# Kernel optimization log

Hardware: AMD Instinct MI355X
Metric: run time of the kernel (lower is better)

Reference implementation:

```python
import jax, jax.numpy as jnp
import numpy as np

D = 1024      # input_dim
H = 16        # head_num
HD = 64       # head_dim
HID = 4096    # mlp hidden
CUR = 512     # cur_seq
PREV = 512    # prev_seq (memory)
FULL = CUR + PREV
BS = 16
SCALE = 1.0 / (HD ** 0.5)


def setup_inputs() -> dict:
    key = jax.random.key(0)
    ks = jax.random.split(key, 20)
    def nrm(k, shape, s=0.02):
        return (jax.random.normal(k, shape) * s).astype(jnp.float32)
    inp = {
        "inputs": nrm(ks[0], (CUR, BS, D), 1.0),
        "pos_embedding": nrm(ks[1], (FULL, 1, D), 1.0),
        "u": nrm(ks[2], (H, HD)),
        "v": nrm(ks[3], (H, HD)),
        "memory": nrm(ks[4], (PREV, BS, D), 1.0),
        # causal mask: position i (query) may attend to j <= i + PREV; True = masked
        "mask": jnp.triu(jnp.ones((CUR, FULL), dtype=bool), k=PREV + 1)[:, :, None],
        # attention params (stored as (in, out); torch Linear applies x @ W.T + b)
        "Wkv": nrm(ks[5], (D, 2 * H * HD)), "bkv": jnp.zeros((2 * H * HD,), jnp.float32),
        "Wq": nrm(ks[6], (D, H * HD)), "bq": jnp.zeros((H * HD,), jnp.float32),
        "Wo": nrm(ks[7], (H * HD, D)), "bo": jnp.zeros((D,), jnp.float32),
        "Wp": nrm(ks[8], (D, H * HD)), "bp": jnp.zeros((H * HD,), jnp.float32),
        # layernorms
        "ln1_g": jnp.ones((D,), jnp.float32), "ln1_b": jnp.zeros((D,), jnp.float32),
        "ln2_g": jnp.ones((D,), jnp.float32), "ln2_b": jnp.zeros((D,), jnp.float32),
        # mlp (mlp_num=2): Linear(D,HID)+relu, Linear(HID,D)+relu
        "W1": nrm(ks[9], (D, HID)), "b1": jnp.zeros((HID,), jnp.float32),
        "W2": nrm(ks[10], (HID, D)), "b2": jnp.zeros((D,), jnp.float32),
        # GRU gates: stacked [Wr,Wz,Wg] and [Ur,Uz,Ug], no bias; bg init 2.0
        "g1_W": nrm(ks[11], (3, D, D)), "g1_U": nrm(ks[12], (3, D, D)),
        "g1_bg": jnp.full((D,), 2.0, jnp.float32),
        "g2_W": nrm(ks[13], (3, D, D)), "g2_U": nrm(ks[14], (3, D, D)),
        "g2_bg": jnp.full((D,), 2.0, jnp.float32),
    }
    return inp


def _layernorm(x, g, b, eps=1e-5):
    mu = jnp.mean(x, axis=-1, keepdims=True)
    var = jnp.mean(jnp.square(x - mu), axis=-1, keepdims=True)
    return (x - mu) * jax.lax.rsqrt(var + eps) * g + b


def _rel_shift(x):
    # x: (bs, head, cur, full) -> pad/reshape/slice trick of Transformer-XL
    b, h, c, f = x.shape
    xp = jnp.pad(x, ((0, 0), (0, 0), (0, 0), (1, 0)))      # (b,h,c,f+1)
    xp = xp.reshape(b, h, f + 1, c)
    return xp[:, :, 1:, :].reshape(b, h, c, f)


def _gru_gate(x, y, W, U, bg):
    # W, U: (3, D, D) for [r, z, g] gates; torch Linear => y @ W[i].T
    r = jax.nn.sigmoid(y @ W[0].T + x @ U[0].T)
    z = jax.nn.sigmoid(y @ W[1].T + x @ U[1].T - bg)
    h = jnp.tanh(y @ W[2].T + (r * x) @ U[2].T)
    return (1.0 - z) * x + z * h


def _attention_xl(x_cur, pos_emb, x_full, u, v, mask,
                  Wkv, bkv, Wq, bq, Wo, bo, Wp, bp):
    cur, bs, _ = x_cur.shape
    full = x_full.shape[0]
    kv = x_full @ Wkv + bkv                                  # (full, bs, 2*H*HD)
    key, value = jnp.split(kv, 2, axis=-1)
    query = x_cur @ Wq + bq                                  # (cur, bs, H*HD)
    r = (pos_emb @ Wp + bp).reshape(full, H, HD)             # (full, H, HD)

    key = key.reshape(full, bs, H, HD)
    value = value.reshape(full, bs, H, HD)
    query = query.reshape(cur, bs, H, HD)

    content = jnp.einsum('ibhd,jbhd->bhij', query + u, key)  # (bs,H,cur,full)
    position = jnp.einsum('ibhd,jhd->bhij', query + v, r)    # (bs,H,cur,full)
    position = _rel_shift(position)

    attn = (content + position) * SCALE
    # mask: (cur, full, 1) bool, True = masked
    m = mask[:, :, 0][None, None]                            # (1,1,cur,full)
    attn = jnp.where(m, -jnp.inf, attn)
    p = jax.nn.softmax(attn, axis=-1)

    out = jnp.einsum('bhij,jbhd->ibhd', p, value).reshape(cur, bs, H * HD)
    return out @ Wo + bo                                     # (cur, bs, D)


def reference(inputs, pos_embedding, u, v, memory, mask,
              Wkv, bkv, Wq, bq, Wo, bo, Wp, bp,
              ln1_g, ln1_b, ln2_g, ln2_b,
              W1, b1, W2, b2,
              g1_W, g1_U, g1_bg, g2_W, g2_U, g2_bg):
    prev = memory.shape[0]
    full_input = jnp.concatenate([memory, inputs], axis=0)   # (full, bs, D)
    x1 = _layernorm(full_input, ln1_g, ln1_b)
    a1 = _attention_xl(x1[prev:], pos_embedding, x1, u, v, mask,
                       Wkv, bkv, Wq, bq, Wo, bo, Wp, bp)
    a1 = jax.nn.relu(a1)                                     # dropout = identity (eval)
    o1 = _gru_gate(inputs, a1, g1_W, g1_U, g1_bg)
    x2 = _layernorm(o1, ln2_g, ln2_b)
    m2 = jax.nn.relu(jax.nn.relu(x2 @ W1 + b1) @ W2 + b2)    # mlp: act after every linear
    o2 = _gru_gate(o1, m2, g2_W, g2_U, g2_bg)
    return o2
```

## Files before the change

kernel.cpp:

```cpp
#include <hip/hip_runtime.h>
#include <stdint.h>

typedef _Float16 h16;
typedef __attribute__((ext_vector_type(8))) _Float16 f16x8;
typedef __attribute__((ext_vector_type(4))) _Float16 f16x4;
typedef __attribute__((ext_vector_type(4))) float f32x4;

enum { F_OBF = 1, F_BIAS = 2, F_RELU = 4, F_ACC = 8, F_DUAL = 16 };

#define BARRIER_MEM                                  \
  do {                                               \
    asm volatile("" ::: "memory");                   \
    __builtin_amdgcn_s_barrier();                    \
    asm volatile("" ::: "memory");                   \
  } while (0)

static __device__ __forceinline__ void gload16(const void* g, void* l) {
  __builtin_amdgcn_global_load_lds((__attribute__((address_space(1))) void*)g,
                                   (__attribute__((address_space(3))) void*)l,
                                   16, 0, 0);
}

template <int FLAGS>
__global__ __launch_bounds__(512) void gemm2_k(
    const h16* __restrict__ A, const h16* __restrict__ B,
    void* __restrict__ Cv, const float* __restrict__ bias,
    int K, int lda, int ldb, int ldc, int gm) {
  __shared__ h16 Al[2][256][64];
  __shared__ h16 Bl[2][256][64];

  const int tid = threadIdx.x, lane = tid & 63, wid = tid >> 6;
  const int wr = wid >> 2, wn = wid & 3;
  const int ar = lane & 15, q4 = lane >> 4;

  const int nwg = gridDim.x, cpx = nwg >> 3;
  const int bid = (blockIdx.x & 7) * cpx + (blockIdx.x >> 3);
  const int mx = bid % gm, ny = bid / gm;

  const h16* Ab = A + (long)mx * 256 * lda;
  const h16* Bb = B + (long)ny * 256 * ldb;

  auto stageA = [&](int buf, int half, int k0) {
#pragma unroll
    for (int l = 0; l < 2; ++l) {
      const int idx = l * 512 + tid;
      const int row = half * 128 + (idx >> 3), sl = idx & 7;
      gload16(Ab + (long)row * lda + k0 + (sl ^ (row & 7)) * 8,
              (char*)&Al[buf][0][0] + (half * 1024 + l * 512 + wid * 64) * 16);
    }
  };
  auto stageB = [&](int buf, int half, int k0) {
#pragma unroll
    for (int l = 0; l < 2; ++l) {
      const int idx = l * 512 + tid;
      const int row = half * 128 + (idx >> 3), sl = idx & 7;
      gload16(Bb + (long)row * ldb + k0 + (sl ^ (row & 7)) * 8,
              (char*)&Bl[buf][0][0] + (half * 1024 + l * 512 + wid * 64) * 16);
    }
  };

  f32x4 acc[8][4] = {};
  const int nk = K >> 6;

  stageB(0, 0, 0); stageB(0, 1, 0); stageA(0, 0, 0); stageA(0, 1, 0);
  if (nk > 1) { stageB(1, 0, 64); stageB(1, 1, 64); stageA(1, 0, 64); stageA(1, 1, 64); }
  if (nk > 1) asm volatile("s_waitcnt vmcnt(8)" ::: "memory");
  else        asm volatile("s_waitcnt vmcnt(0)" ::: "memory");
  BARRIER_MEM;

  for (int kt = 0; kt < nk; ++kt) {
    const int b = kt & 1;
    const int k2 = (kt + 2) << 6;
    const bool pf = (kt + 2) < nk;

    f16x8 a0[4][2], b0[2][2];
#pragma unroll
    for (int m = 0; m < 4; ++m) {
      const int row = wr * 128 + m * 16 + ar;
#pragma unroll
      for (int ks = 0; ks < 2; ++ks)
        a0[m][ks] = *(const f16x8*)&Al[b][row][((ks * 4 + q4) ^ (row & 7)) * 8];
    }
#pragma unroll
    for (int n = 0; n < 2; ++n) {
      const int row = wn * 64 + n * 16 + ar;
#pragma unroll
      for (int ks = 0; ks < 2; ++ks)
        b0[n][ks] = *(const f16x8*)&Bl[b][row][((ks * 4 + q4) ^ (row & 7)) * 8];
    }
    BARRIER_MEM;
    __builtin_amdgcn_s_setprio(1);
#pragma unroll
    for (int m = 0; m < 4; ++m)
#pragma unroll
      for (int n = 0; n < 2; ++n)
#pragma unroll
        for (int ks = 0; ks < 2; ++ks)
          acc[m][n] = __builtin_amdgcn_mfma_f32_16x16x32_f16(a0[m][ks], b0[n][ks], acc[m][n], 0, 0, 0);
    __builtin_amdgcn_s_setprio(0);
    BARRIER_MEM;

    f16x8 b1f[2][2];
#pragma unroll
    for (int n = 0; n < 2; ++n) {
      const int row = wn * 64 + (n + 2) * 16 + ar;
#pragma unroll
      for (int ks = 0; ks < 2; ++ks)
        b1f[n][ks] = *(const f16x8*)&Bl[b][row][((ks * 4 + q4) ^ (row & 7)) * 8];
    }
    BARRIER_MEM;
    __builtin_amdgcn_s_setprio(1);
#pragma unroll
    for (int m = 0; m < 4; ++m)
#pragma unroll
      for (int n = 0; n < 2; ++n)
#pragma unroll
        for (int ks = 0; ks < 2; ++ks)
          acc[m][n + 2] = __builtin_amdgcn_mfma_f32_16x16x32_f16(a0[m][ks], b1f[n][ks], acc[m][n + 2], 0, 0, 0);
    __builtin_amdgcn_s_setprio(0);
    BARRIER_MEM;

    f16x8 a1f[4][2];
#pragma unroll
    for (int m = 0; m < 4; ++m) {
      const int row = wr * 128 + (m + 4) * 16 + ar;
#pragma unroll
      for (int ks = 0; ks < 2; ++ks)
        a1f[m][ks] = *(const f16x8*)&Al[b][row][((ks * 4 + q4) ^ (row & 7)) * 8];
    }
    if (pf) { stageB(b, 0, k2); stageB(b, 1, k2); }
    BARRIER_MEM;
    __builtin_amdgcn_s_setprio(1);
#pragma unroll
    for (int m = 0; m < 4; ++m)
#pragma unroll
      for (int n = 0; n < 2; ++n)
#pragma unroll
        for (int ks = 0; ks < 2; ++ks)
          acc[m + 4][n] = __builtin_amdgcn_mfma_f32_16x16x32_f16(a1f[m][ks], b0[n][ks], acc[m + 4][n], 0, 0, 0);
    __builtin_amdgcn_s_setprio(0);
    BARRIER_MEM;

    if (pf) { stageA(b, 0, k2); stageA(b, 1, k2); }
    __builtin_amdgcn_s_setprio(1);
#pragma unroll
    for (int m = 0; m < 4; ++m)
#pragma unroll
      for (int n = 0; n < 2; ++n)
#pragma unroll
        for (int ks = 0; ks < 2; ++ks)
          acc[m + 4][n + 2] = __builtin_amdgcn_mfma_f32_16x16x32_f16(a1f[m][ks], b1f[n][ks], acc[m + 4][n + 2], 0, 0, 0);
    __builtin_amdgcn_s_setprio(0);
    if (pf)                 asm volatile("s_waitcnt vmcnt(8)" ::: "memory");
    else if (kt + 1 < nk)   asm volatile("s_waitcnt vmcnt(0)" ::: "memory");
    BARRIER_MEM;
  }

#pragma unroll
  for (int m = 0; m < 8; ++m) {
#pragma unroll
    for (int n = 0; n < 4; ++n) {
      const int col = ny * 256 + wn * 64 + n * 16 + ar;
      float bv1 = 0.f;
      if (FLAGS & F_BIAS) bv1 = bias[col];
#pragma unroll
      for (int r = 0; r < 4; ++r) {
        const int row = mx * 256 + wr * 128 + m * 16 + q4 * 4 + r;
        float val = acc[m][n][r] + bv1;
        if (FLAGS & F_RELU) val = fmaxf(val, 0.f);
        if constexpr ((FLAGS & F_ACC) != 0) {
          float* p = (float*)Cv + (long)row * ldc + col;
          *p = *p + val;
        } else if constexpr ((FLAGS & F_OBF) != 0) {
          ((h16*)Cv)[(long)row * ldc + col] = (h16)val;
        } else {
          ((float*)Cv)[(long)row * ldc + col] = val;
        }
      }
    }
  }
}

template <int BM, int BN, int WAVES_M, int WAVES_N, int FLAGS>
__global__ __launch_bounds__(256) void gemm_k(
    const h16* __restrict__ A, const h16* __restrict__ B,
    void* __restrict__ Cv, void* __restrict__ C2v,
    const float* __restrict__ bias, const float* __restrict__ bias2,
    int K, int lda, int ldb, int ldc,
    long sAb, long sAh, long sBb, long sBh, long sCb, long sCh) {
  constexpr int BK = 32;
  constexpr int WM = BM / WAVES_M, WN = BN / WAVES_N;
  constexpr int MF = WM / 16, NF = WN / 16;
  constexpr int LPS = BM / 64 + BN / 64;
  __shared__ h16 Al[3][BM][BK];
  __shared__ h16 Bl[3][BN][BK];

  const int tid = threadIdx.x, lane = tid & 63, wid = tid >> 6;
  const int wm = wid / WAVES_N, wn = wid % WAVES_N;
  const int z = blockIdx.z, zb = z >> 4, zh = z & 15;
  const h16* Ab = A + zb * sAb + zh * sAh + (long)blockIdx.x * BM * lda;
  const h16* Bb = B + zb * sBb + zh * sBh + (long)blockIdx.y * BN * ldb;

  const int srow = lane >> 2;
  const int skc = (((lane & 3) ^ ((lane >> 3) & 3)) * 8);

  auto stage = [&](int buf, int k0) {
#pragma unroll
    for (int t = 0; t < BM / 64; ++t) {
      const int ii = wid + t * 4;
      gload16(Ab + (long)(ii * 16 + srow) * lda + k0 + skc, &Al[buf][ii * 16][0]);
    }
#pragma unroll
    for (int t = 0; t < BN / 64; ++t) {
      const int ii = wid + t * 4;
      gload16(Bb + (long)(ii * 16 + srow) * ldb + k0 + skc, &Bl[buf][ii * 16][0]);
    }
  };

  f32x4 acc[MF][NF] = {};
  const int nk = K / BK;
  const int ar = lane & 15, ls = lane >> 4;

  stage(0, 0);
  if (nk > 1) stage(1, BK);
  for (int kt = 0; kt < nk; ++kt) {
    if (kt == nk - 1) {
      asm volatile("s_waitcnt vmcnt(0)" ::: "memory");
    } else if constexpr (LPS == 4) {
      asm volatile("s_waitcnt vmcnt(4)" ::: "memory");
    } else if constexpr (LPS == 3) {
      asm volatile("s_waitcnt vmcnt(3)" ::: "memory");
    } else {
      asm volatile("s_waitcnt vmcnt(0)" ::: "memory");
    }
    __builtin_amdgcn_s_barrier();
    asm volatile("" ::: "memory");
    if (kt + 2 < nk) stage((kt + 2) % 3, (kt + 2) * BK);
    const int cur = kt % 3;
    f16x8 af[MF], bv[NF];
#pragma unroll
    for (int m = 0; m < MF; ++m) {
      const int R = wm * WM + m * 16 + ar;
      af[m] = *(const f16x8*)&Al[cur][R][(ls ^ ((R >> 1) & 3)) * 8];
    }
#pragma unroll
    for (int n = 0; n < NF; ++n) {
      const int R = wn * WN + n * 16 + ar;
      bv[n] = *(const f16x8*)&Bl[cur][R][(ls ^ ((R >> 1) & 3)) * 8];
    }
#pragma unroll
    for (int m = 0; m < MF; ++m)
#pragma unroll
      for (int n = 0; n < NF; ++n)
        acc[m][n] = __builtin_amdgcn_mfma_f32_16x16x32_f16(af[m], bv[n], acc[m][n], 0, 0, 0);
  }

  const long coff = (long)zb * sCb + (long)zh * sCh;
#pragma unroll
  for (int m = 0; m < MF; ++m) {
#pragma unroll
    for (int n = 0; n < NF; ++n) {
      const int col = blockIdx.y * BN + wn * WN + n * 16 + ar;
      float bv1 = 0.f, bv2 = 0.f;
      if (FLAGS & F_BIAS) bv1 = bias[col];
      if (FLAGS & F_DUAL) bv2 = bias2[col];
#pragma unroll
      for (int r = 0; r < 4; ++r) {
        const int row = blockIdx.x * BM + wm * WM + m * 16 + (lane >> 4) * 4 + r;
        float val = acc[m][n][r] + bv1;
        if (FLAGS & F_RELU) val = fmaxf(val, 0.f);
        if constexpr ((FLAGS & F_ACC) != 0) {
          float* p = (float*)Cv + coff + (long)row * ldc + col;
          *p = *p + val;
        } else if constexpr ((FLAGS & F_OBF) != 0) {
          ((h16*)Cv)[coff + (long)row * ldc + col] = (h16)val;
          if constexpr ((FLAGS & F_DUAL) != 0)
            ((h16*)C2v)[coff + (long)row * ldc + col] = (h16)(acc[m][n][r] + bv2);
        } else {
          ((float*)Cv)[coff + (long)row * ldc + col] = val;
        }
      }
    }
  }
}

__global__ __launch_bounds__(256) void fattn_k(
    const h16* __restrict__ qu, const h16* __restrict__ qv,
    const h16* __restrict__ kvb, const h16* __restrict__ vT,
    const h16* __restrict__ rb, h16* __restrict__ attn) {
  __shared__ h16 Kl[128][64];
  __shared__ h16 Vl[64][128];
  __shared__ h16 Psc[4][16][164];

  const int tid = threadIdx.x, lane = tid & 63, wv = tid >> 6;
  const int z = blockIdx.x, b = z >> 4, h = z & 15;
  const int i0 = blockIdx.y * 64;
  const int ar = lane & 15, q4 = lane >> 4;
  const int myrow = i0 + wv * 16;

  const long qoff = ((long)(myrow + ar) * 16 + b) * 1024 + h * 64 + q4 * 8;
  f16x8 quf[2], qvf[2];
  quf[0] = *(const f16x8*)&qu[qoff];
  quf[1] = *(const f16x8*)&qu[qoff + 32];
  qvf[0] = *(const f16x8*)&qv[qoff];
  qvf[1] = *(const f16x8*)&qv[qoff + 32];

  f32x4 o[4] = {};
  float mrow[4], lrow[4];
#pragma unroll
  for (int r = 0; r < 4; ++r) { mrow[r] = -3e38f; lrow[r] = 0.f; }

  const int ntiles = (i0 + 575 + 128) >> 7;

  for (int t = 0; t < ntiles; ++t) {
    const int j0 = t * 128;
    __builtin_amdgcn_s_barrier();
#pragma unroll
    for (int it = 0; it < 4; ++it) {
      const int ch = it * 256 + wv * 64 + lane;
      const int kr = ch >> 3, ks = ch & 7;
      gload16(kvb + ((long)(j0 + kr) * 16 + b) * 2048 + h * 64 + (ks ^ (kr & 7)) * 8,
              (char*)&Kl[0][0] + (it * 256 + wv * 64) * 16);
    }
#pragma unroll
    for (int it = 0; it < 4; ++it) {
      const int ch = it * 256 + wv * 64 + lane;
      const int vd = ch >> 4, vs = ch & 15;
      gload16(vT + ((long)z * 64 + vd) * 1024 + j0 + (vs ^ (vd & 7)) * 8,
              (char*)&Vl[0][0] + (it * 256 + wv * 64) * 16);
    }
    asm volatile("s_waitcnt vmcnt(0)" ::: "memory");
    __builtin_amdgcn_s_barrier();

    f32x4 acc_c[8] = {};
#pragma unroll
    for (int kd = 0; kd < 2; ++kd)
#pragma unroll
      for (int nf = 0; nf < 8; ++nf) {
        const int j = nf * 16 + ar;
        const int phys = (kd * 4 + q4) ^ (j & 7);
        const f16x8 kf = *(const f16x8*)&Kl[j][phys * 8];
        acc_c[nf] = __builtin_amdgcn_mfma_f32_16x16x32_f16(quf[kd], kf, acc_c[nf], 0, 0, 0);
      }

    const int jbase = j0 - myrow + 496;
    f32x4 acc_p[9] = {};
#pragma unroll
    for (int kd = 0; kd < 2; ++kd)
#pragma unroll
      for (int jf = 0; jf < 9; ++jf) {
        int jjr = jbase + jf * 16 + ar;
        if (jjr > 1023) jjr = 1023;
        const f16x8 rf = *(const f16x8*)&rb[(long)jjr * 1024 + h * 64 + kd * 32 + q4 * 8];
        acc_p[jf] = __builtin_amdgcn_mfma_f32_16x16x32_f16(qvf[kd], rf, acc_p[jf], 0, 0, 0);
      }
#pragma unroll
    for (int jf = 0; jf < 9; ++jf)
#pragma unroll
      for (int r = 0; r < 4; ++r)
        Psc[wv][q4 * 4 + r][jf * 16 + ar] = (h16)acc_p[jf][r];

    float p[8][4];
#pragma unroll
    for (int nf = 0; nf < 8; ++nf)
#pragma unroll
      for (int r = 0; r < 4; ++r) {
        const int iloc = q4 * 4 + r;
        const int jloc = nf * 16 + ar;
        const int band = jloc - iloc + 15;
        const float pv = (float)Psc[wv][iloc][band];
        float sv = (acc_c[nf][r] + pv) * 0.125f;
        const bool ok = (j0 + jloc) <= (myrow + iloc + 512);
        p[nf][r] = ok ? sv : -3e38f;
      }
#pragma unroll
    for (int r = 0; r < 4; ++r) {
      float tm = -3e38f;
#pragma unroll
      for (int nf = 0; nf < 8; ++nf) tm = fmaxf(tm, p[nf][r]);
      tm = fmaxf(tm, __shfl_xor(tm, 1));
      tm = fmaxf(tm, __shfl_xor(tm, 2));
      tm = fmaxf(tm, __shfl_xor(tm, 4));
      tm = fmaxf(tm, __shfl_xor(tm, 8));
      const float mn = fmaxf(mrow[r], tm);
      const float sc = __expf(mrow[r] - mn);
      mrow[r] = mn;
      float ts = 0.f;
#pragma unroll
      for (int nf = 0; nf < 8; ++nf) {
        const float e = __expf(p[nf][r] - mn);
        p[nf][r] = e;
        ts += e;
      }
      ts += __shfl_xor(ts, 1);
      ts += __shfl_xor(ts, 2);
      ts += __shfl_xor(ts, 4);
      ts += __shfl_xor(ts, 8);
      lrow[r] = lrow[r] * sc + ts;
#pragma unroll
      for (int v = 0; v < 4; ++v) o[v][r] *= sc;
    }

#pragma unroll
    for (int nf = 0; nf < 8; ++nf)
#pragma unroll
      for (int r = 0; r < 4; ++r) {
        const int iloc = q4 * 4 + r, jloc = nf * 16 + ar;
        Psc[wv][iloc][((jloc >> 3) ^ (iloc & 7)) * 8 + (jloc & 7)] = (h16)p[nf][r];
      }
#pragma unroll
    for (int ks = 0; ks < 4; ++ks) {
      const f16x8 pa = *(const f16x8*)&Psc[wv][ar][((ks * 4 + q4) ^ (ar & 7)) * 8];
#pragma unroll
      for (int vnf = 0; vnf < 4; ++vnf) {
        const int d = vnf * 16 + ar;
        const f16x8 vb = *(const f16x8*)&Vl[d][((ks * 4 + q4) ^ (d & 7)) * 8];
        o[vnf] = __builtin_amdgcn_mfma_f32_16x16x32_f16(pa, vb, o[vnf], 0, 0, 0);
      }
    }
  }

#pragma unroll
  for (int vnf = 0; vnf < 4; ++vnf)
#pragma unroll
    for (int r = 0; r < 4; ++r) {
      const int i_ = myrow + q4 * 4 + r;
      attn[((long)i_ * 16 + b) * 1024 + h * 64 + vnf * 16 + ar] =
          (h16)(o[vnf][r] / lrow[r]);
    }
}

__global__ __launch_bounds__(256) void wtrans_k(const float* __restrict__ in,
                                                h16* __restrict__ out, int K, int N) {
  __shared__ float t[32][33];
  const int tx = threadIdx.x & 31, ty = threadIdx.x >> 5;
  const int n0 = blockIdx.x * 32, k0 = blockIdx.y * 32;
#pragma unroll
  for (int j = 0; j < 32; j += 8)
    t[ty + j][tx] = in[(long)(k0 + ty + j) * N + n0 + tx];
  __syncthreads();
#pragma unroll
  for (int j = 0; j < 32; j += 8)
    out[(long)(n0 + ty + j) * K + k0 + tx] = (h16)t[tx][ty + j];
}

__global__ __launch_bounds__(256) void cast_k(const float* __restrict__ in,
                                              h16* __restrict__ out, long n4) {
  const long i = (long)blockIdx.x * 256 + threadIdx.x;
  if (i >= n4) return;
  const float4 v = ((const float4*)in)[i];
  f16x4 o;
  o[0] = (h16)v.x; o[1] = (h16)v.y; o[2] = (h16)v.z; o[3] = (h16)v.w;
  ((f16x4*)out)[i] = o;
}

__global__ void addbias_k(const float* __restrict__ bq, const float* __restrict__ u,
                          const float* __restrict__ v, float* __restrict__ qu,
                          float* __restrict__ qv) {
  const int c = blockIdx.x * 256 + threadIdx.x;
  if (c < 1024) { qu[c] = bq[c] + u[c]; qv[c] = bq[c] + v[c]; }
}

__global__ __launch_bounds__(256) void zero_out_k(float* __restrict__ out, long n) {
  const long i = (long)blockIdx.x * 256 + threadIdx.x;
  if (i < n) out[i] = 0.f;
}

__global__ __launch_bounds__(256) void ln_k(const float* __restrict__ src0,
                                            const float* __restrict__ src1, int rows0,
                                            const float* __restrict__ g,
                                            const float* __restrict__ b,
                                            h16* __restrict__ out) {
  const int row = blockIdx.x, tid = threadIdx.x;
  const float* src = (row < rows0) ? (src0 + (long)row * 1024)
                                   : (src1 + (long)(row - rows0) * 1024);
  const float4 x = ((const float4*)src)[tid];
  float s = x.x + x.y + x.z + x.w;
  float sq = x.x * x.x + x.y * x.y + x.z * x.z + x.w * x.w;
#pragma unroll
  for (int o = 32; o > 0; o >>= 1) { s += __shfl_down(s, o); sq += __shfl_down(sq, o); }
  __shared__ float red[8];
  const int lane = tid & 63, w = tid >> 6;
  if (lane == 0) { red[w] = s; red[4 + w] = sq; }
  __syncthreads();
  s = red[0] + red[1] + red[2] + red[3];
  sq = red[4] + red[5] + red[6] + red[7];
  const float mu = s * (1.f / 1024.f);
  const float inv = rsqrtf(sq * (1.f / 1024.f) - mu * mu + 1e-5f);
  const float4 gg = ((const float4*)g)[tid], bb = ((const float4*)b)[tid];
  f16x4 o;
  o[0] = (h16)((x.x - mu) * inv * gg.x + bb.x);
  o[1] = (h16)((x.y - mu) * inv * gg.y + bb.y);
  o[2] = (h16)((x.z - mu) * inv * gg.z + bb.z);
  o[3] = (h16)((x.w - mu) * inv * gg.w + bb.w);
  ((f16x4*)(out + (long)row * 1024))[tid] = o;
}

__global__ __launch_bounds__(256) void vtrans_k(const h16* __restrict__ kv,
                                                h16* __restrict__ vT) {
  const int z = blockIdx.y, b = z >> 4, h = z & 15;
  const int j0 = blockIdx.x * 64;
  __shared__ h16 t[64][72];
  const int jj = threadIdx.x >> 3, c = threadIdx.x & 7;
#pragma unroll
  for (int half = 0; half < 2; ++half) {
    const int j = jj + half * 32;
    const f16x8 v = *(const f16x8*)(kv + ((long)(j0 + j) * 16 + b) * 2048 + 1024 + h * 64 + c * 8);
    *(f16x8*)&t[j][c * 8] = v;
  }
  __syncthreads();
#pragma unroll
  for (int half = 0; half < 2; ++half) {
    const int d = jj + half * 32;
    f16x8 o;
#pragma unroll
    for (int k = 0; k < 8; ++k) o[k] = t[c * 8 + k][d];
    *(f16x8*)(vT + ((long)z * 64 + d) * 1024 + j0 + c * 8) = o;
  }
}

__global__ __launch_bounds__(256) void gru_rx_k(const float* __restrict__ T,
                                                const float* __restrict__ x,
                                                h16* __restrict__ rx) {
  const long i = (long)blockIdx.x * 256 + threadIdx.x;
  const long row = i >> 8;
  const int c4 = (int)(i & 255);
  const float4 t = *((const float4*)(T + row * 3072) + c4);
  const float4 xx = ((const float4*)x)[i];
  f16x4 o;
  o[0] = (h16)(xx.x / (1.f + __expf(-t.x)));
  o[1] = (h16)(xx.y / (1.f + __expf(-t.y)));
  o[2] = (h16)(xx.z / (1.f + __expf(-t.z)));
  o[3] = (h16)(xx.w / (1.f + __expf(-t.w)));
  ((f16x4*)rx)[i] = o;
}

__global__ __launch_bounds__(256) void gru_out_k(const float* __restrict__ T,
                                                 const float* __restrict__ x,
                                                 const float* __restrict__ bg,
                                                 float* __restrict__ outf,
                                                 h16* __restrict__ outh) {
  const long i = (long)blockIdx.x * 256 + threadIdx.x;
  const long row = i >> 8;
  const int c4 = (int)(i & 255);
  const float4 tz = *((const float4*)(T + row * 3072 + 1024) + c4);
  const float4 th = *((const float4*)(T + row * 3072 + 2048) + c4);
  const float4 xx = ((const float4*)x)[i];
  const float4 bb = ((const float4*)bg)[c4];
  float4 o;
  {
    const float z0 = 1.f / (1.f + __expf(-(tz.x - bb.x)));
    const float z1 = 1.f / (1.f + __expf(-(tz.y - bb.y)));
    const float z2 = 1.f / (1.f + __expf(-(tz.z - bb.z)));
    const float z3 = 1.f / (1.f + __expf(-(tz.w - bb.w)));
    o.x = (1.f - z0) * xx.x + z0 * tanhf(th.x);
    o.y = (1.f - z1) * xx.y + z1 * tanhf(th.y);
    o.z = (1.f - z2) * xx.z + z2 * tanhf(th.z);
    o.w = (1.f - z3) * xx.w + z3 * tanhf(th.w);
  }
  ((float4*)outf)[i] = o;
  if (outh != nullptr) {
    f16x4 oh;
    oh[0] = (h16)o.x; oh[1] = (h16)o.y; oh[2] = (h16)o.z; oh[3] = (h16)o.w;
    ((f16x4*)outh)[i] = oh;
  }
}

extern "C" void kernel_launch(void* const* d_in, const int* in_sizes, int n_in,
                              void* d_out, int out_size, void* d_ws, size_t ws_size,
                              hipStream_t stream) {
  const float* inputs = (const float*)d_in[0];
  const float* pos    = (const float*)d_in[1];
  const float* u      = (const float*)d_in[2];
  const float* v      = (const float*)d_in[3];
  const float* memory = (const float*)d_in[4];
  const float* Wkv = (const float*)d_in[6];  const float* bkv = (const float*)d_in[7];
  const float* Wq  = (const float*)d_in[8];  const float* bq  = (const float*)d_in[9];
  const float* Wo  = (const float*)d_in[10]; const float* bo  = (const float*)d_in[11];
  const float* Wp  = (const float*)d_in[12]; const float* bp  = (const float*)d_in[13];
  const float* ln1_g = (const float*)d_in[14]; const float* ln1_b = (const float*)d_in[15];
  const float* ln2_g = (const float*)d_in[16]; const float* ln2_b = (const float*)d_in[17];
  const float* W1 = (const float*)d_in[18]; const float* b1 = (const float*)d_in[19];
  const float* W2 = (const float*)d_in[20]; const float* b2 = (const float*)d_in[21];
  const float* g1_W = (const float*)d_in[22]; const float* g1_U = (const float*)d_in[23];
  const float* g1_bg = (const float*)d_in[24];
  const float* g2_W = (const float*)d_in[25]; const float* g2_U = (const float*)d_in[26];
  const float* g2_bg = (const float*)d_in[27];
  (void)in_sizes; (void)n_in;

  const size_t MB = 1u << 20;
  const size_t NEEDED = 247 * MB;
  const dim3 blk(256);
  if (ws_size < NEEDED) {
    zero_out_k<<<(out_size + 255) / 256, blk, 0, stream>>>((float*)d_out, out_size);
    return;
  }

  char* w = (char*)d_ws;
  h16* WoT   = (h16*)(w + 0 * MB);
  h16* W1T   = (h16*)(w + 2 * MB);
  h16* W2T   = (h16*)(w + 10 * MB);
  h16* g1Wb  = (h16*)(w + 18 * MB);
  h16* g1Ub  = (h16*)(w + 24 * MB);
  h16* g2Wb  = (h16*)(w + 30 * MB);
  h16* g2Ub  = (h16*)(w + 36 * MB);
  h16* WkvT  = (h16*)(w + 42 * MB);
  h16* WqT   = (h16*)(w + 46 * MB);
  h16* WpT   = (h16*)(w + 48 * MB);
  h16* posb  = (h16*)(w + 50 * MB);
  float* bias_qu = (float*)(w + 52 * MB);
  float* bias_qv = (float*)(w + 52 * MB + 8192);
  h16* xb    = (h16*)(w + 53 * MB);
  h16* x1    = (h16*)(w + 69 * MB);
  char* Rbig =        w + 101 * MB;
  h16* qu    = (h16*)(w + 197 * MB);
  h16* qv    = (h16*)(w + 213 * MB);
  h16* rb    = (h16*)(w + 229 * MB);
  h16* attn  = (h16*)(w + 231 * MB);

  h16*   kvb  = (h16*)Rbig;
  float* Tall = (float*)Rbig;
  h16*   h1   = (h16*)Rbig;
  h16*   vT   = x1;
  h16*   a1   = qu;
  h16*   rx1  = qv;
  float* o1f  = (float*)qu;
  h16*   o1b  = attn;
  h16*   x2   = x1;
  h16*   m2   = x1 + 8L * 1024 * 1024;
  h16*   rx2  = x1;

  wtrans_k<<<dim3(64, 32), blk, 0, stream>>>(Wkv, WkvT, 1024, 2048);
  wtrans_k<<<dim3(32, 32), blk, 0, stream>>>(Wq, WqT, 1024, 1024);
  wtrans_k<<<dim3(32, 32), blk, 0, stream>>>(Wo, WoT, 1024, 1024);
  wtrans_k<<<dim3(32, 32), blk, 0, stream>>>(Wp, WpT, 1024, 1024);
  wtrans_k<<<dim3(128, 32), blk, 0, stream>>>(W1, W1T, 1024, 4096);
  wtrans_k<<<dim3(32, 128), blk, 0, stream>>>(W2, W2T, 4096, 1024);
  cast_k<<<3072, blk, 0, stream>>>(g1_W, g1Wb, 786432);
  cast_k<<<3072, blk, 0, stream>>>(g1_U, g1Ub, 786432);
  cast_k<<<3072, blk, 0, stream>>>(g2_W, g2Wb, 786432);
  cast_k<<<3072, blk, 0, stream>>>(g2_U, g2Ub, 786432);
  cast_k<<<1024, blk, 0, stream>>>(pos, posb, 262144);
  cast_k<<<8192, blk, 0, stream>>>(inputs, xb, 2097152);
  addbias_k<<<4, blk, 0, stream>>>(bq, u, v, bias_qu, bias_qv);

  ln_k<<<16384, blk, 0, stream>>>(memory, inputs, 8192, ln1_g, ln1_b, x1);

  gemm2_k<F_OBF | F_BIAS><<<dim3(512), dim3(512), 0, stream>>>(
      x1, WkvT, kvb, bkv, 1024, 1024, 1024, 2048, 64);
  gemm_k<64, 128, 2, 2, F_OBF | F_BIAS | F_DUAL><<<dim3(128, 8, 1), blk, 0, stream>>>(
      x1 + 8192L * 1024, WqT, qu, qv, bias_qu, bias_qv, 1024, 1024, 1024, 1024, 0, 0, 0, 0, 0, 0);
  gemm_k<128, 128, 2, 2, F_OBF | F_BIAS><<<dim3(8, 8, 1), blk, 0, stream>>>(
      posb, WpT, rb, nullptr, bp, nullptr, 1024, 1024, 1024, 1024, 0, 0, 0, 0, 0, 0);
  vtrans_k<<<dim3(16, 256), blk, 0, stream>>>(kvb, vT);

  fattn_k<<<dim3(256, 8), blk, 0, stream>>>(qu, qv, kvb, vT, rb, attn);

  gemm_k<64, 128, 2, 2, F_OBF | F_BIAS | F_RELU><<<dim3(128, 8, 1), blk, 0, stream>>>(
      attn, WoT, a1, nullptr, bo, nullptr, 1024, 1024, 1024, 1024, 0, 0, 0, 0, 0, 0);

  gemm2_k<0><<<dim3(384), dim3(512), 0, stream>>>(
      a1, g1Wb, Tall, nullptr, 1024, 1024, 1024, 3072, 32);
  gemm2_k<F_ACC><<<dim3(256), dim3(512), 0, stream>>>(
      xb, g1Ub, Tall, nullptr, 1024, 1024, 1024, 3072, 32);
  gru_rx_k<<<8192, blk, 0, stream>>>(Tall, inputs, rx1);
  gemm_k<64, 128, 2, 2, F_ACC><<<dim3(128, 8, 1), blk, 0, stream>>>(
      rx1, g1Ub + 2L * 1024 * 1024, Tall + 2048, nullptr, nullptr, nullptr,
      1024, 1024, 1024, 3072, 0, 0, 0, 0, 0, 0);
  gru_out_k<<<8192, blk, 0, stream>>>(Tall, inputs, g1_bg, o1f, o1b);

  ln_k<<<8192, blk, 0, stream>>>(o1f, o1f, 8192, ln2_g, ln2_b, x2);
  gemm2_k<F_OBF | F_BIAS | F_RELU><<<dim3(512), dim3(512), 0, stream>>>(
      x2, W1T, h1, b1, 1024, 1024, 1024, 4096, 32);
  gemm_k<64, 128, 2, 2, F_OBF | F_BIAS | F_RELU><<<dim3(128, 8, 1), blk, 0, stream>>>(
      h1, W2T, m2, nullptr, b2, nullptr, 4096, 4096, 4096, 1024, 0, 0, 0, 0, 0, 0);

  gemm2_k<0><<<dim3(384), dim3(512), 0, stream>>>(
      m2, g2Wb, Tall, nullptr, 1024, 1024, 1024, 3072, 32);
  gemm2_k<F_ACC><<<dim3(256), dim3(512), 0, stream>>>(
      o1b, g2Ub, Tall, nullptr, 1024, 1024, 1024, 3072, 32);
  gru_rx_k<<<8192, blk, 0, stream>>>(Tall, o1f, rx2);
  gemm_k<64, 128, 2, 2, F_ACC><<<dim3(128, 8, 1), blk, 0, stream>>>(
      rx2, g2Ub + 2L * 1024 * 1024, Tall + 2048, nullptr, nullptr, nullptr,
      1024, 1024, 1024, 3072, 0, 0, 0, 0, 0, 0);
  gru_out_k<<<8192, blk, 0, stream>>>(Tall, o1f, g2_bg, (float*)d_out, nullptr);
}
```

Measured before the change: 1.133 ms.

## Template gemm2_k on BN and route all N=1024 GEMMs through it; drop V LDS staging

Adds a BN template parameter (128 or 256) to the 256x256 8-wave GEMM kernel and uses the 256x128 variant for every N=1024 projection (Q, pos, Wo, W2, GRU candidate), removing the older 256-thread gemm_k. The dual-output Q GEMM becomes two separate launches that each recompute the same product with a different bias. In the attention kernel the V tile is now read directly from global memory instead of being staged in LDS, which saves LDS and a staging pass but makes the PV MFMA operands depend on global/cache latency. The pos GEMM launches only 32 workgroups, which may underfill the GPU.

```diff
diff --git a/kernel.cpp b/kernel.cpp
--- a/kernel.cpp
+++ b/kernel.cpp
@@ -6,7 +6,7 @@
 typedef __attribute__((ext_vector_type(4))) _Float16 f16x4;
 typedef __attribute__((ext_vector_type(4))) float f32x4;
 
-enum { F_OBF = 1, F_BIAS = 2, F_RELU = 4, F_ACC = 8, F_DUAL = 16 };
+enum { F_OBF = 1, F_BIAS = 2, F_RELU = 4, F_ACC = 8 };
 
 #define BARRIER_MEM                                  \
   do {                                               \
@@ -21,13 +21,15 @@
                                    16, 0, 0);
 }
 
-template <int FLAGS>
+template <int BN, int FLAGS>
 __global__ __launch_bounds__(512) void gemm2_k(
     const h16* __restrict__ A, const h16* __restrict__ B,
     void* __restrict__ Cv, const float* __restrict__ bias,
     int K, int lda, int ldb, int ldc, int gm) {
+  constexpr int NH = BN / 128;
+  constexpr int WN = BN / 4;
   __shared__ h16 Al[2][256][64];
-  __shared__ h16 Bl[2][256][64];
+  __shared__ h16 Bl[2][BN][64];
 
   const int tid = threadIdx.x, lane = tid & 63, wid = tid >> 6;
   const int wr = wid >> 2, wn = wid & 3;
@@ -38,7 +40,7 @@
   const int mx = bid % gm, ny = bid / gm;
 
   const h16* Ab = A + (long)mx * 256 * lda;
-  const h16* Bb = B + (long)ny * 256 * ldb;
+  const h16* Bb = B + (long)ny * BN * ldb;
 
   auto stageA = [&](int buf, int half, int k0) {
 #pragma unroll
@@ -51,21 +53,25 @@
   };
   auto stageB = [&](int buf, int half, int k0) {
 #pragma unroll
-    for (int l = 0; l < 2; ++l) {
+    for (int l = 0; l < NH; ++l) {
       const int idx = l * 512 + tid;
-      const int row = half * 128 + (idx >> 3), sl = idx & 7;
+      const int row = half * (BN / 2) + (idx >> 3), sl = idx & 7;
       gload16(Bb + (long)row * ldb + k0 + (sl ^ (row & 7)) * 8,
-              (char*)&Bl[buf][0][0] + (half * 1024 + l * 512 + wid * 64) * 16);
+              (char*)&Bl[buf][0][0] + (half * (BN * 4) + l * 512 + wid * 64) * 16);
     }
   };
 
-  f32x4 acc[8][4] = {};
+  f32x4 acc[8][2 * NH] = {};
   const int nk = K >> 6;
 
   stageB(0, 0, 0); stageB(0, 1, 0); stageA(0, 0, 0); stageA(0, 1, 0);
   if (nk > 1) { stageB(1, 0, 64); stageB(1, 1, 64); stageA(1, 0, 64); stageA(1, 1, 64); }
-  if (nk > 1) asm volatile("s_waitcnt vmcnt(8)" ::: "memory");
-  else        asm volatile("s_waitcnt vmcnt(0)" ::: "memory");
+  if (nk > 1) {
+    if constexpr (NH == 2) asm volatile("s_waitcnt vmcnt(8)" ::: "memory");
+    else                   asm volatile("s_waitcnt vmcnt(6)" ::: "memory");
+  } else {
+    asm volatile("s_waitcnt vmcnt(0)" ::: "memory");
+  }
   BARRIER_MEM;
 
   for (int kt = 0; kt < nk; ++kt) {
@@ -73,7 +79,7 @@
     const int k2 = (kt + 2) << 6;
     const bool pf = (kt + 2) < nk;
 
-    f16x8 a0[4][2], b0[2][2];
+    f16x8 a0[4][2], b0[NH][2];
 #pragma unroll
     for (int m = 0; m < 4; ++m) {
       const int row = wr * 128 + m * 16 + ar;
@@ -82,8 +88,8 @@
         a0[m][ks] = *(const f16x8*)&Al[b][row][((ks * 4 + q4) ^ (row & 7)) * 8];
     }
 #pragma unroll
-    for (int n = 0; n < 2; ++n) {
-      const int row = wn * 64 + n * 16 + ar;
+    for (int n = 0; n < NH; ++n) {
+      const int row = wn * WN + n * 16 + ar;
 #pragma unroll
       for (int ks = 0; ks < 2; ++ks)
         b0[n][ks] = *(const f16x8*)&Bl[b][row][((ks * 4 + q4) ^ (row & 7)) * 8];
@@ -93,17 +99,17 @@
 #pragma unroll
     for (int m = 0; m < 4; ++m)
 #pragma unroll
-      for (int n = 0; n < 2; ++n)
+      for (int n = 0; n < NH; ++n)
 #pragma unroll
         for (int ks = 0; ks < 2; ++ks)
           acc[m][n] = __builtin_amdgcn_mfma_f32_16x16x32_f16(a0[m][ks], b0[n][ks], acc[m][n], 0, 0, 0);
     __builtin_amdgcn_s_setprio(0);
     BARRIER_MEM;
 
-    f16x8 b1f[2][2];
-#pragma unroll
-    for (int n = 0; n < 2; ++n) {
-      const int row = wn * 64 + (n + 2) * 16 + ar;
+    f16x8 b1f[NH][2];
+#pragma unroll
+    for (int n = 0; n < NH; ++n) {
+      const int row = wn * WN + (n + NH) * 16 + ar;
 #pragma unroll
       for (int ks = 0; ks < 2; ++ks)
         b1f[n][ks] = *(const f16x8*)&Bl[b][row][((ks * 4 + q4) ^ (row & 7)) * 8];
@@ -113,10 +119,10 @@
 #pragma unroll
     for (int m = 0; m < 4; ++m)
 #pragma unroll
-      for (int n = 0; n < 2; ++n)
+      for (int n = 0; n < NH; ++n)
 #pragma unroll
         for (int ks = 0; ks < 2; ++ks)
-          acc[m][n + 2] = __builtin_amdgcn_mfma_f32_16x16x32_f16(a0[m][ks], b1f[n][ks], acc[m][n + 2], 0, 0, 0);
+          acc[m][n + NH] = __builtin_amdgcn_mfma_f32_16x16x32_f16(a0[m][ks], b1f[n][ks], acc[m][n + NH], 0, 0, 0);
     __builtin_amdgcn_s_setprio(0);
     BARRIER_MEM;
 
@@ -134,7 +140,7 @@
 #pragma unroll
     for (int m = 0; m < 4; ++m)
 #pragma unroll
-      for (int n = 0; n < 2; ++n)
+      for (int n = 0; n < NH; ++n)
 #pragma unroll
         for (int ks = 0; ks < 2; ++ks)
           acc[m + 4][n] = __builtin_amdgcn_mfma_f32_16x16x32_f16(a1f[m][ks], b0[n][ks], acc[m + 4][n], 0, 0, 0);
@@ -146,21 +152,25 @@
 #pragma unroll
     for (int m = 0; m < 4; ++m)
 #pragma unroll
-      for (int n = 0; n < 2; ++n)
+      for (int n = 0; n < NH; ++n)
 #pragma unroll
         for (int ks = 0; ks < 2; ++ks)
-          acc[m + 4][n + 2] = __builtin_amdgcn_mfma_f32_16x16x32_f16(a1f[m][ks], b1f[n][ks], acc[m + 4][n + 2], 0, 0, 0);
+          acc[m + 4][n + NH] = __builtin_amdgcn_mfma_f32_16x16x32_f16(a1f[m][ks], b1f[n][ks], acc[m + 4][n + NH], 0, 0, 0);
     __builtin_amdgcn_s_setprio(0);
-    if (pf)                 asm volatile("s_waitcnt vmcnt(8)" ::: "memory");
-    else if (kt + 1 < nk)   asm volatile("s_waitcnt vmcnt(0)" ::: "memory");
+    if (pf) {
+      if constexpr (NH == 2) asm volatile("s_waitcnt vmcnt(8)" ::: "memory");
+      else                   asm volatile("s_waitcnt vmcnt(6)" ::: "memory");
+    } else if (kt + 1 < nk) {
+      asm volatile("s_waitcnt vmcnt(0)" ::: "memory");
+    }
     BARRIER_MEM;
   }
 
 #pragma unroll
   for (int m = 0; m < 8; ++m) {
 #pragma unroll
-    for (int n = 0; n < 4; ++n) {
-      const int col = ny * 256 + wn * 64 + n * 16 + ar;
+    for (int n = 0; n < 2 * NH; ++n) {
+      const int col = ny * BN + wn * WN + n * 16 + ar;
       float bv1 = 0.f;
       if (FLAGS & F_BIAS) bv1 = bias[col];
 #pragma unroll
@@ -181,115 +191,11 @@
   }
 }
 
-template <int BM, int BN, int WAVES_M, int WAVES_N, int FLAGS>
-__global__ __launch_bounds__(256) void gemm_k(
-    const h16* __restrict__ A, const h16* __restrict__ B,
-    void* __restrict__ Cv, void* __restrict__ C2v,
-    const float* __restrict__ bias, const float* __restrict__ bias2,
-    int K, int lda, int ldb, int ldc,
-    long sAb, long sAh, long sBb, long sBh, long sCb, long sCh) {
-  constexpr int BK = 32;
-  constexpr int WM = BM / WAVES_M, WN = BN / WAVES_N;
-  constexpr int MF = WM / 16, NF = WN / 16;
-  constexpr int LPS = BM / 64 + BN / 64;
-  __shared__ h16 Al[3][BM][BK];
-  __shared__ h16 Bl[3][BN][BK];
-
-  const int tid = threadIdx.x, lane = tid & 63, wid = tid >> 6;
-  const int wm = wid / WAVES_N, wn = wid % WAVES_N;
-  const int z = blockIdx.z, zb = z >> 4, zh = z & 15;
-  const h16* Ab = A + zb * sAb + zh * sAh + (long)blockIdx.x * BM * lda;
-  const h16* Bb = B + zb * sBb + zh * sBh + (long)blockIdx.y * BN * ldb;
-
-  const int srow = lane >> 2;
-  const int skc = (((lane & 3) ^ ((lane >> 3) & 3)) * 8);
-
-  auto stage = [&](int buf, int k0) {
-#pragma unroll
-    for (int t = 0; t < BM / 64; ++t) {
-      const int ii = wid + t * 4;
-      gload16(Ab + (long)(ii * 16 + srow) * lda + k0 + skc, &Al[buf][ii * 16][0]);
-    }
-#pragma unroll
-    for (int t = 0; t < BN / 64; ++t) {
-      const int ii = wid + t * 4;
-      gload16(Bb + (long)(ii * 16 + srow) * ldb + k0 + skc, &Bl[buf][ii * 16][0]);
-    }
-  };
-
-  f32x4 acc[MF][NF] = {};
-  const int nk = K / BK;
-  const int ar = lane & 15, ls = lane >> 4;
-
-  stage(0, 0);
-  if (nk > 1) stage(1, BK);
-  for (int kt = 0; kt < nk; ++kt) {
-    if (kt == nk - 1) {
-      asm volatile("s_waitcnt vmcnt(0)" ::: "memory");
-    } else if constexpr (LPS == 4) {
-      asm volatile("s_waitcnt vmcnt(4)" ::: "memory");
-    } else if constexpr (LPS == 3) {
-      asm volatile("s_waitcnt vmcnt(3)" ::: "memory");
-    } else {
-      asm volatile("s_waitcnt vmcnt(0)" ::: "memory");
-    }
-    __builtin_amdgcn_s_barrier();
-    asm volatile("" ::: "memory");
-    if (kt + 2 < nk) stage((kt + 2) % 3, (kt + 2) * BK);
-    const int cur = kt % 3;
-    f16x8 af[MF], bv[NF];
-#pragma unroll
-    for (int m = 0; m < MF; ++m) {
-      const int R = wm * WM + m * 16 + ar;
-      af[m] = *(const f16x8*)&Al[cur][R][(ls ^ ((R >> 1) & 3)) * 8];
-    }
-#pragma unroll
-    for (int n = 0; n < NF; ++n) {
-      const int R = wn * WN + n * 16 + ar;
-      bv[n] = *(const f16x8*)&Bl[cur][R][(ls ^ ((R >> 1) & 3)) * 8];
-    }
-#pragma unroll
-    for (int m = 0; m < MF; ++m)
-#pragma unroll
-      for (int n = 0; n < NF; ++n)
-        acc[m][n] = __builtin_amdgcn_mfma_f32_16x16x32_f16(af[m], bv[n], acc[m][n], 0, 0, 0);
-  }
-
-  const long coff = (long)zb * sCb + (long)zh * sCh;
-#pragma unroll
-  for (int m = 0; m < MF; ++m) {
-#pragma unroll
-    for (int n = 0; n < NF; ++n) {
-      const int col = blockIdx.y * BN + wn * WN + n * 16 + ar;
-      float bv1 = 0.f, bv2 = 0.f;
-      if (FLAGS & F_BIAS) bv1 = bias[col];
-      if (FLAGS & F_DUAL) bv2 = bias2[col];
-#pragma unroll
-      for (int r = 0; r < 4; ++r) {
-        const int row = blockIdx.x * BM + wm * WM + m * 16 + (lane >> 4) * 4 + r;
-        float val = acc[m][n][r] + bv1;
-        if (FLAGS & F_RELU) val = fmaxf(val, 0.f);
-        if constexpr ((FLAGS & F_ACC) != 0) {
-          float* p = (float*)Cv + coff + (long)row * ldc + col;
-          *p = *p + val;
-        } else if constexpr ((FLAGS & F_OBF) != 0) {
-          ((h16*)Cv)[coff + (long)row * ldc + col] = (h16)val;
-          if constexpr ((FLAGS & F_DUAL) != 0)
-            ((h16*)C2v)[coff + (long)row * ldc + col] = (h16)(acc[m][n][r] + bv2);
-        } else {
-          ((float*)Cv)[coff + (long)row * ldc + col] = val;
-        }
-      }
-    }
-  }
-}
-
 __global__ __launch_bounds__(256) void fattn_k(
     const h16* __restrict__ qu, const h16* __restrict__ qv,
     const h16* __restrict__ kvb, const h16* __restrict__ vT,
     const h16* __restrict__ rb, h16* __restrict__ attn) {
   __shared__ h16 Kl[128][64];
-  __shared__ h16 Vl[64][128];
   __shared__ h16 Psc[4][16][164];
 
   const int tid = threadIdx.x, lane = tid & 63, wv = tid >> 6;
@@ -297,6 +203,7 @@
   const int i0 = blockIdx.y * 64;
   const int ar = lane & 15, q4 = lane >> 4;
   const int myrow = i0 + wv * 16;
+  const h16* vTz = vT + (long)z * 64 * 1024;
 
   const long qoff = ((long)(myrow + ar) * 16 + b) * 1024 + h * 64 + q4 * 8;
   f16x8 quf[2], qvf[2];
@@ -321,13 +228,6 @@
       const int kr = ch >> 3, ks = ch & 7;
       gload16(kvb + ((long)(j0 + kr) * 16 + b) * 2048 + h * 64 + (ks ^ (kr & 7)) * 8,
               (char*)&Kl[0][0] + (it * 256 + wv * 64) * 16);
-    }
-#pragma unroll
-    for (int it = 0; it < 4; ++it) {
-      const int ch = it * 256 + wv * 64 + lane;
-      const int vd = ch >> 4, vs = ch & 15;
-      gload16(vT + ((long)z * 64 + vd) * 1024 + j0 + (vs ^ (vd & 7)) * 8,
-              (char*)&Vl[0][0] + (it * 256 + wv * 64) * 16);
     }
     asm volatile("s_waitcnt vmcnt(0)" ::: "memory");
     __builtin_amdgcn_s_barrier();
@@ -414,7 +314,7 @@
 #pragma unroll
       for (int vnf = 0; vnf < 4; ++vnf) {
         const int d = vnf * 16 + ar;
-        const f16x8 vb = *(const f16x8*)&Vl[d][((ks * 4 + q4) ^ (d & 7)) * 8];
+        const f16x8 vb = *(const f16x8*)&vTz[(long)d * 1024 + j0 + ks * 32 + q4 * 8];
         o[vnf] = __builtin_amdgcn_mfma_f32_16x16x32_f16(pa, vb, o[vnf], 0, 0, 0);
       }
     }
@@ -646,42 +546,42 @@
 
   ln_k<<<16384, blk, 0, stream>>>(memory, inputs, 8192, ln1_g, ln1_b, x1);
 
-  gemm2_k<F_OBF | F_BIAS><<<dim3(512), dim3(512), 0, stream>>>(
+  gemm2_k<256, F_OBF | F_BIAS><<<dim3(512), dim3(512), 0, stream>>>(
       x1, WkvT, kvb, bkv, 1024, 1024, 1024, 2048, 64);
-  gemm_k<64, 128, 2, 2, F_OBF | F_BIAS | F_DUAL><<<dim3(128, 8, 1), blk, 0, stream>>>(
-      x1 + 8192L * 1024, WqT, qu, qv, bias_qu, bias_qv, 1024, 1024, 1024, 1024, 0, 0, 0, 0, 0, 0);
-  gemm_k<128, 128, 2, 2, F_OBF | F_BIAS><<<dim3(8, 8, 1), blk, 0, stream>>>(
-      posb, WpT, rb, nullptr, bp, nullptr, 1024, 1024, 1024, 1024, 0, 0, 0, 0, 0, 0);
+  gemm2_k<128, F_OBF | F_BIAS><<<dim3(256), dim3(512), 0, stream>>>(
+      x1 + 8192L * 1024, WqT, qu, bias_qu, 1024, 1024, 1024, 1024, 32);
+  gemm2_k<128, F_OBF | F_BIAS><<<dim3(256), dim3(512), 0, stream>>>(
+      x1 + 8192L * 1024, WqT, qv, bias_qv, 1024, 1024, 1024, 1024, 32);
+  gemm2_k<128, F_OBF | F_BIAS><<<dim3(32), dim3(512), 0, stream>>>(
+      posb, WpT, rb, bp, 1024, 1024, 1024, 1024, 4);
   vtrans_k<<<dim3(16, 256), blk, 0, stream>>>(kvb, vT);
 
   fattn_k<<<dim3(256, 8), blk, 0, stream>>>(qu, qv, kvb, vT, rb, attn);
 
-  gemm_k<64, 128, 2, 2, F_OBF | F_BIAS | F_RELU><<<dim3(128, 8, 1), blk, 0, stream>>>(
-      attn, WoT, a1, nullptr, bo, nullptr, 1024, 1024, 1024, 1024, 0, 0, 0, 0, 0, 0);
-
-  gemm2_k<0><<<dim3(384), dim3(512), 0, stream>>>(
+  gemm2_k<128, F_OBF | F_BIAS | F_RELU><<<dim3(256), dim3(512), 0, stream>>>(
+      attn, WoT, a1, bo, 1024, 1024, 1024, 1024, 32);
+
+  gemm2_k<256, 0><<<dim3(384), dim3(512), 0, stream>>>(
       a1, g1Wb, Tall, nullptr, 1024, 1024, 1024, 3072, 32);
-  gemm2_k<F_ACC><<<dim3(256), dim3(512), 0, stream>>>(
+  gemm2_k<256, F_ACC><<<dim3(256), dim3(512), 0, stream>>>(
       xb, g1Ub, Tall, nullptr, 1024, 1024, 1024, 3072, 32);
   gru_rx_k<<<8192, blk, 0, stream>>>(Tall, inputs, rx1);
-  gemm_k<64, 128, 2, 2, F_ACC><<<dim3(128, 8, 1), blk, 0, stream>>>(
-      rx1, g1Ub + 2L * 1024 * 1024, Tall + 2048, nullptr, nullptr, nullptr,
-      1024, 1024, 1024, 3072, 0, 0, 0, 0, 0, 0);
+  gemm2_k<128, F_ACC><<<dim3(256), dim3(512), 0, stream>>>(
+      rx1, g1Ub + 2L * 1024 * 1024, Tall + 2048, nullptr, 1024, 1024, 1024, 3072, 32);
   gru_out_k<<<8192, blk, 0, stream>>>(Tall, inputs, g1_bg, o1f, o1b);
 
   ln_k<<<8192, blk, 0, stream>>>(o1f, o1f, 8192, ln2_g, ln2_b, x2);
-  gemm2_k<F_OBF | F_BIAS | F_RELU><<<dim3(512), dim3(512), 0, stream>>>(
+  gemm2_k<256, F_OBF | F_BIAS | F_RELU><<<dim3(512), dim3(512), 0, stream>>>(
       x2, W1T, h1, b1, 1024, 1024, 1024, 4096, 32);
-  gemm_k<64, 128, 2, 2, F_OBF | F_BIAS | F_RELU><<<dim3(128, 8, 1), blk, 0, stream>>>(
-      h1, W2T, m2, nullptr, b2, nullptr, 4096, 4096, 4096, 1024, 0, 0, 0, 0, 0, 0);
-
-  gemm2_k<0><<<dim3(384), dim3(512), 0, stream>>>(
+  gemm2_k<128, F_OBF | F_BIAS | F_RELU><<<dim3(256), dim3(512), 0, stream>>>(
+      h1, W2T, m2, b2, 4096, 4096, 4096, 1024, 32);
+
+  gemm2_k<256, 0><<<dim3(384), dim3(512), 0, stream>>>(
       m2, g2Wb, Tall, nullptr, 1024, 1024, 1024, 3072, 32);
-  gemm2_k<F_ACC><<<dim3(256), dim3(512), 0, stream>>>(
+  gemm2_k<256, F_ACC><<<dim3(256), dim3(512), 0, stream>>>(
       o1b, g2Ub, Tall, nullptr, 1024, 1024, 1024, 3072, 32);
   gru_rx_k<<<8192, blk, 0, stream>>>(Tall, o1f, rx2);
-  gemm_k<64, 128, 2, 2, F_ACC><<<dim3(128, 8, 1), blk, 0, stream>>>(
-      rx2, g2Ub + 2L * 1024 * 1024, Tall + 2048, nullptr, nullptr, nullptr,
-      1024, 1024, 1024, 3072, 0, 0, 0, 0, 0, 0);
+  gemm2_k<128, F_ACC><<<dim3(256), dim3(512), 0, stream>>>(
+      rx2, g2Ub + 2L * 1024 * 1024, Tall + 2048, nullptr, 1024, 1024, 1024, 3072, 32);
   gru_out_k<<<8192, blk, 0, stream>>>(Tall, o1f, g2_bg, (float*)d_out, nullptr);
 }
```

Result: slower. 1.203 ms (+6.2%).
